# Performance work log

Measured on AMD Instinct MI355X. Metric: run time of the kernel, lower is better.

The kernel has to match this reference:

```python
import jax, jax.numpy as jnp
import numpy as np

B, H, K = 4096, 256, 16
INPUT_DIM, XPRIME_DIM = 8, 64
D = INPUT_DIM * XPRIME_DIM  # 512
LN_EPS = 1e-5


def setup_inputs() -> dict:
    key = jax.random.key(0)
    ks = jax.random.split(key, 12)
    s1 = 1.0  # Linear(1, D): fan_in=1
    sD = 1.0 / np.sqrt(D)
    sH = 1.0 / np.sqrt(H)
    return {
        "h_prev_rnn": jax.random.normal(ks[0], (B, H), jnp.float32),
        "x_l": jax.random.normal(ks[1], (B, INPUT_DIM), jnp.float32),
        "x_ext": jax.random.normal(ks[2], (B, K), jnp.float32),
        # stacked per-expert MetaNet params
        "meta_w1": jax.random.uniform(ks[3], (K, D), jnp.float32, -s1, s1),
        "meta_b1": jax.random.uniform(ks[4], (K, D), jnp.float32, -s1, s1),
        "meta_w2": jax.random.uniform(ks[5], (K, D, D), jnp.float32, -sD, sD),
        "meta_b2": jax.random.uniform(ks[6], (K, D), jnp.float32, -sD, sD),
        # gating net
        "gw1": jax.random.uniform(ks[7], (H, H), jnp.float32, -sH, sH),
        "gb1": jax.random.uniform(ks[8], (H,), jnp.float32, -sH, sH),
        "gw2": jax.random.uniform(ks[9], (H, K), jnp.float32, -sH, sH),
        "gb2": jax.random.uniform(ks[10], (K,), jnp.float32, -sH, sH),
        # LayerNorm([input_dim, xprime_dim]) affine params
        "ln_g": jnp.ones((INPUT_DIM, XPRIME_DIM), jnp.float32),
        "ln_b": jnp.zeros((INPUT_DIM, XPRIME_DIM), jnp.float32),
        "theta0": jnp.zeros((1, INPUT_DIM, XPRIME_DIM), jnp.float32),
    }


def reference(h_prev_rnn, x_l, x_ext, meta_w1, meta_b1, meta_w2, meta_b2,
              gw1, gb1, gw2, gb2, ln_g, ln_b, theta0):
    # MetaNet layer1 (Linear(1, D)): scalar input per expert -> [B, K, D]
    h1 = jnp.tanh(x_ext[:, :, None] * meta_w1[None] + meta_b1[None])
    # MetaNet layer2: per-expert DxD GEMM
    h2 = jnp.tanh(jnp.einsum('bkd,kde->bke', h1, meta_w2) + meta_b2[None])
    W = h2.reshape(h2.shape[0], K, INPUT_DIM, XPRIME_DIM)  # [B,K,i,e]
    # LayerNorm over last two dims jointly, affine
    mu = W.mean(axis=(-2, -1), keepdims=True)
    var = W.var(axis=(-2, -1), keepdims=True)
    W = (W - mu) * jax.lax.rsqrt(var + LN_EPS) * ln_g + ln_b
    # gating: softmax over experts (epoch/top_k = None path)
    logits = jnp.tanh(h_prev_rnn @ gw1 + gb1) @ gw2 + gb2
    gates = jax.nn.softmax(logits, axis=-1)  # [B, K]
    theta = jnp.einsum('bk,bkie->bie', gates, W) + theta0  # [B, i, e]
    x_prime = jnp.einsum('bi,bie->be', x_l, theta)  # [B, e]
    return (x_prime, theta)
```

## Files before the change

kernel.cpp:

```cpp
#include <hip/hip_runtime.h>
#include <stdint.h>

#define NB 4096
#define NH 256
#define NK 16
#define ND 512
#define NC 48
#define NM 48
#define RCHEB 7.0f
#define PI_F 3.14159265358979323846f
#define CCPART (NK * 2 * ND * 32)

typedef _Float16 f16;
using half8   = __attribute__((ext_vector_type(8))) _Float16;
using float4v = __attribute__((ext_vector_type(4))) float;

__device__ __forceinline__ float fast_tanh(float x) {
  float e = __builtin_amdgcn_exp2f(x * 2.88539008177793f);
  return 1.0f - 2.0f * __builtin_amdgcn_rcpf(e + 1.0f);
}

template <int CTRL>
__device__ __forceinline__ float dpp_addstep(float x) {
  int y = __builtin_amdgcn_update_dpp(0, __builtin_bit_cast(int, x),
                                      CTRL, 0xf, 0xf, true);
  return x + __builtin_bit_cast(float, y);
}
__device__ __forceinline__ float rowsum16(float x) {
  x = dpp_addstep<0xB1>(x);
  x = dpp_addstep<0x4E>(x);
  x = dpp_addstep<0x141>(x);
  x = dpp_addstep<0x140>(x);
  return x;
}

__global__ __launch_bounds__(256) void k_gs(
    const float* __restrict__ h_prev,
    const float* __restrict__ gw1, const float* __restrict__ gb1,
    const float* __restrict__ gw2, const float* __restrict__ gb2,
    const float* __restrict__ w1, const float* __restrict__ b1,
    float* __restrict__ gates, float* __restrict__ Sg, float* __restrict__ ctg) {
  __shared__ __align__(16) float sbuf[8288];
  const int t = threadIdx.x;
  const int blk = blockIdx.x;

  if (blk >= 512) {
    const int sb = blk - 512;
    const int k = sb >> 3;
    const int d0 = (sb & 7) * 64;
    if (sb == 0) {
      for (int i = t; i < NM * NC; i += 256) {
        const int m = i / 48, j = i - m * 48;
        const int r = (j * (2 * m + 1)) % 192;
        const float fac = (j == 0 ? 1.0f : 2.0f) * (1.0f / 48.0f);
        ctg[i] = cosf(PI_F * (float)r * (1.0f / 96.0f)) * fac;
      }
    }
    const int dl = t >> 2, mg = t & 3;
    const int d = d0 + dl;
    const float a = w1[k * ND + d];
    const float b = b1[k * ND + d];
    float o[12];
#pragma unroll
    for (int mi = 0; mi < 12; ++mi) {
      const int m = mg * 12 + mi;
      const float cx = cosf(PI_F * (float)(2 * m + 1) * (1.0f / 96.0f));
      o[mi] = fast_tanh(fmaf(a, RCHEB * cx, b));
    }
    float* dst = Sg + ((size_t)k * ND + d) * NM + mg * 12;
    *(float4*)&dst[0] = *(float4*)&o[0];
    *(float4*)&dst[4] = *(float4*)&o[4];
    *(float4*)&dst[8] = *(float4*)&o[8];
    return;
  }

  float* sh_h = sbuf;
  float* sh_t = sbuf + 2048;
  float* gw2t = sbuf + 4128;
  const int b0 = blk * 8;
  for (int r = 0; r < 8; ++r) sh_h[r * 256 + t] = h_prev[(b0 + r) * NH + t];
  {
    float4 gr[4];
#pragma unroll
    for (int i4 = 0; i4 < 4; ++i4) gr[i4] = *(const float4*)&gw2[t * NK + i4 * 4];
#pragma unroll
    for (int kk = 0; kk < 16; ++kk) gw2t[kk * 260 + t] = ((const float*)gr)[kk];
  }
  __syncthreads();
  float acc[8];
  const float bias = gb1[t];
#pragma unroll
  for (int r = 0; r < 8; ++r) acc[r] = bias;
  for (int i = 0; i < NH; i += 4) {
    const float w0 = gw1[(i + 0) * NH + t];
    const float w1v = gw1[(i + 1) * NH + t];
    const float w2v = gw1[(i + 2) * NH + t];
    const float w3 = gw1[(i + 3) * NH + t];
#pragma unroll
    for (int r = 0; r < 8; ++r) {
      const float4 hv = *(const float4*)&sh_h[r * 256 + i];
      acc[r] += hv.x * w0 + hv.y * w1v + hv.z * w2v + hv.w * w3;
    }
  }
#pragma unroll
  for (int r = 0; r < 8; ++r) sh_t[r * 260 + t] = fast_tanh(acc[r]);
  __syncthreads();
  if (t < 128) {
    const int r = t >> 4, k = t & 15;
    float lg = gb2[k];
#pragma unroll 8
    for (int j4 = 0; j4 < 64; ++j4) {
      const float4 tv = *(const float4*)&sh_t[r * 260 + j4 * 4];
      const float4 wv = *(const float4*)&gw2t[k * 260 + j4 * 4];
      lg += tv.x * wv.x + tv.y * wv.y + tv.z * wv.z + tv.w * wv.w;
    }
    float m = lg;
    for (int off = 1; off < 16; off <<= 1) m = fmaxf(m, __shfl_xor(m, off, 16));
    const float e = __builtin_amdgcn_exp2f((lg - m) * 1.44269504f);
    float s = e;
    for (int off = 1; off < 16; off <<= 1) s += __shfl_xor(s, off, 16);
    gates[(b0 + r) * NK + k] = e * __builtin_amdgcn_rcpf(s);
  }
}

__global__ __launch_bounds__(256) void k_coef(
    const float* __restrict__ w2, const float* __restrict__ Sg,
    const float* __restrict__ ctg, float* __restrict__ Cc) {
  __shared__ float Gl[48][68];
  const int t = threadIdx.x;
  const int blk = blockIdx.x;
  const int k = blk >> 5;
  const int e0 = ((blk >> 2) & 7) * 64;
  const int dq = blk & 3;
  const int el = t & 63;
  const int mqu = __builtin_amdgcn_readfirstlane(t >> 6);

  const float* w2p = w2 + ((size_t)k * ND + dq * 128) * ND + e0 + el;
  const float* Sp = Sg + ((size_t)k * ND + dq * 128) * NM + mqu * 12;

  float g[12];
#pragma unroll
  for (int i = 0; i < 12; ++i) g[i] = 0.f;
#pragma unroll 4
  for (int d = 0; d < 128; ++d) {
    const float wv = w2p[(size_t)d * ND];
    const float4 s0 = *(const float4*)&Sp[d * NM];
    const float4 s1 = *(const float4*)&Sp[d * NM + 4];
    const float4 s2 = *(const float4*)&Sp[d * NM + 8];
    g[0] = fmaf(s0.x, wv, g[0]);
    g[1] = fmaf(s0.y, wv, g[1]);
    g[2] = fmaf(s0.z, wv, g[2]);
    g[3] = fmaf(s0.w, wv, g[3]);
    g[4] = fmaf(s1.x, wv, g[4]);
    g[5] = fmaf(s1.y, wv, g[5]);
    g[6] = fmaf(s1.z, wv, g[6]);
    g[7] = fmaf(s1.w, wv, g[7]);
    g[8] = fmaf(s2.x, wv, g[8]);
    g[9] = fmaf(s2.y, wv, g[9]);
    g[10] = fmaf(s2.z, wv, g[10]);
    g[11] = fmaf(s2.w, wv, g[11]);
  }

#pragma unroll
  for (int mi = 0; mi < 12; ++mi) Gl[mqu * 12 + mi][el] = g[mi];
  __syncthreads();

  float cacc[12];
#pragma unroll
  for (int i = 0; i < 12; ++i) cacc[i] = 0.f;
#pragma unroll 4
  for (int m = 0; m < NM; ++m) {
    const float gv = Gl[m][el];
    const float4 c0 = *(const float4*)&ctg[m * 48 + mqu * 12];
    const float4 c1 = *(const float4*)&ctg[m * 48 + mqu * 12 + 4];
    const float4 c2 = *(const float4*)&ctg[m * 48 + mqu * 12 + 8];
    cacc[0] = fmaf(c0.x, gv, cacc[0]);
    cacc[1] = fmaf(c0.y, gv, cacc[1]);
    cacc[2] = fmaf(c0.z, gv, cacc[2]);
    cacc[3] = fmaf(c0.w, gv, cacc[3]);
    cacc[4] = fmaf(c1.x, gv, cacc[4]);
    cacc[5] = fmaf(c1.y, gv, cacc[5]);
    cacc[6] = fmaf(c1.z, gv, cacc[6]);
    cacc[7] = fmaf(c1.w, gv, cacc[7]);
    cacc[8] = fmaf(c2.x, gv, cacc[8]);
    cacc[9] = fmaf(c2.y, gv, cacc[9]);
    cacc[10] = fmaf(c2.z, gv, cacc[10]);
    cacc[11] = fmaf(c2.w, gv, cacc[11]);
  }
  float* Ccq = Cc + (size_t)dq * CCPART;
#pragma unroll
  for (int jj = 0; jj < 12; ++jj) {
    const int j = mqu * 12 + jj;
    Ccq[((size_t)(k * 2 + (j >> 5)) * ND + e0 + el) * 32 + (j & 31)] = cacc[jj];
  }
}

__global__ __launch_bounds__(256) void k_pack(
    const float* __restrict__ Cc, const float* __restrict__ b2,
    f16* __restrict__ Cbf) {
  const int idx = blockIdx.x * 256 + threadIdx.x;
  const int flat8 = idx * 8;
  const int k2 = flat8 >> 14;
  const int rem = flat8 & 16383;
  const int e = rem >> 5, o8 = rem & 31;
  const int j0 = (k2 & 1) * 32 + o8;
  f16 o[8];
  if (j0 >= 48) {
#pragma unroll
    for (int i = 0; i < 8; ++i) o[i] = (f16)0.f;
  } else {
    float v[8];
#pragma unroll
    for (int i = 0; i < 8; ++i) v[i] = 0.f;
#pragma unroll
    for (int p = 0; p < 4; ++p) {
      const float4 u0 = *(const float4*)&Cc[(size_t)p * CCPART + flat8];
      const float4 u1 = *(const float4*)&Cc[(size_t)p * CCPART + flat8 + 4];
      v[0] += u0.x; v[1] += u0.y; v[2] += u0.z; v[3] += u0.w;
      v[4] += u1.x; v[5] += u1.y; v[6] += u1.z; v[7] += u1.w;
    }
    if (((k2 & 1) == 0) && (o8 == 0)) v[0] += b2[(k2 >> 1) * ND + e];
#pragma unroll
    for (int i = 0; i < 8; ++i) o[i] = (f16)v[i];
  }
  *(uint4*)&Cbf[flat8] = *(uint4*)o;
}

__global__ __launch_bounds__(512) void k_eval(
    const f16* __restrict__ Cbf, const float* __restrict__ gates,
    const float* __restrict__ x_ext, const float* __restrict__ x_l,
    const float* __restrict__ ln_g, const float* __restrict__ ln_b,
    const float* __restrict__ theta0, float* __restrict__ out) {
  __shared__ __align__(16) char sm[40960];
  f16* Tlds = (f16*)sm;
  float (*xp)[16][68] = (float(*)[16][68])sm;
  float* lnbuf = (float*)(sm + 36864);
  float* scal  = (float*)(sm + 38144);
  float (*sx)[16] = (float(*)[16])(sm + 38400);
  float (*sg)[16] = (float(*)[16])(sm + 39424);
  float (*sxl)[8] = (float(*)[8])(sm + 40448);
  const int t = threadIdx.x;
  const int l = t & 63, wn = t >> 6;
  const int q = l >> 4, m16 = l & 15;
  const int b0 = blockIdx.x * 16;

  const f16* Bbase = Cbf + ((size_t)(wn * 64 + m16)) * 32 + q * 8;
  half8 BrA[8], BrB[8];
  auto loadB = [&](int k, half8(&dst)[8]) {
#pragma unroll
    for (int bni = 0; bni < 4; ++bni) {
      dst[bni * 2 + 0] =
          *(const half8*)(Bbase + ((size_t)(k * 2 + 0) * ND + bni * 16) * 32);
      dst[bni * 2 + 1] =
          *(const half8*)(Bbase + ((size_t)(k * 2 + 1) * ND + bni * 16) * 32);
    }
  };
  loadB(0, BrA);

  if (t < 256) {
    sx[t >> 4][t & 15] = x_ext[(b0 + (t >> 4)) * NK + (t & 15)];
    sg[t >> 4][t & 15] = gates[(b0 + (t >> 4)) * NK + (t & 15)];
  } else if (t < 384) {
    const int tt = t - 256;
    sxl[tt >> 3][tt & 7] = x_l[(b0 + (tt >> 3)) * 8 + (tt & 7)];
  }
  __syncthreads();

  if (t < 256) {
    const int k = t >> 4, row = t & 15;
    f16* T0 = &Tlds[(2 * k) * 576 + row * 36];
    f16* T1 = &Tlds[(2 * k + 1) * 576 + row * 36];
    float u = sx[row][k] * (1.0f / RCHEB);
    u = fminf(1.0f, fmaxf(-1.0f, u));
    const float u2 = u + u;
    float tp = 1.0f, tc = u;
    T0[0] = (f16)1.0f;
    T0[1] = (f16)u;
#pragma unroll
    for (int j = 2; j < 48; ++j) {
      const float tn = fmaf(u2, tc, -tp);
      tp = tc; tc = tn;
      if (j < 32) T0[j] = (f16)tn; else T1[j - 32] = (f16)tn;
    }
#pragma unroll
    for (int j = 48; j < 64; ++j) T1[j - 32] = (f16)0.f;
  }
  __syncthreads();

  float lng[4], lnb[4];
#pragma unroll
  for (int bni = 0; bni < 4; ++bni) {
    const int col = wn * 64 + bni * 16 + m16;
    lng[bni] = ln_g[col];
    lnb[bni] = ln_b[col];
  }

  float th[4][4];
#pragma unroll
  for (int bni = 0; bni < 4; ++bni)
#pragma unroll
    for (int rr = 0; rr < 4; ++rr) th[bni][rr] = 0.f;

  const f16* Abase = Tlds + m16 * 36 + q * 8;
  const float4v z = {0.f, 0.f, 0.f, 0.f};

  float4v acc[4];
  float s[4], s2[4];

  auto stepA = [&](int k, const half8(&Br)[8]) {
    const half8 a0 = *(const half8*)(Abase + (2 * k) * 576);
    const half8 a1 = *(const half8*)(Abase + (2 * k + 1) * 576);
#pragma unroll
    for (int bni = 0; bni < 4; ++bni) {
      acc[bni] = __builtin_amdgcn_mfma_f32_16x16x32_f16(a0, Br[2 * bni], z, 0, 0, 0);
      acc[bni] = __builtin_amdgcn_mfma_f32_16x16x32_f16(a1, Br[2 * bni + 1],
                                                        acc[bni], 0, 0, 0);
    }
#pragma unroll
    for (int rr = 0; rr < 4; ++rr) { s[rr] = 0.f; s2[rr] = 0.f; }
#pragma unroll
    for (int bni = 0; bni < 4; ++bni)
#pragma unroll
      for (int rr = 0; rr < 4; ++rr) {
        const float v = fast_tanh(acc[bni][rr]);
        acc[bni][rr] = v;
        s[rr] += v;
        s2[rr] = fmaf(v, v, s2[rr]);
      }
#pragma unroll
    for (int rr = 0; rr < 4; ++rr) {
      s[rr] = rowsum16(s[rr]);
      s2[rr] = rowsum16(s2[rr]);
    }
    if (m16 == 0) {
#pragma unroll
      for (int rr = 0; rr < 4; ++rr)
        *(float2*)&lnbuf[(q * 4 + rr) * 20 + wn * 2] = make_float2(s[rr], s2[rr]);
    }
  };
  auto scalc = [&](int k) {
    if (wn == 0 && l < 16) {
      const int row = l;
      const float4 p0 = *(const float4*)&lnbuf[row * 20 + 0];
      const float4 p1 = *(const float4*)&lnbuf[row * 20 + 4];
      const float4 p2 = *(const float4*)&lnbuf[row * 20 + 8];
      const float4 p3 = *(const float4*)&lnbuf[row * 20 + 12];
      const float S1 = p0.x + p0.z + p1.x + p1.z + p2.x + p2.z + p3.x + p3.z;
      const float S2 = p0.y + p0.w + p1.y + p1.w + p2.y + p2.w + p3.y + p3.w;
      const float mu = S1 * (1.0f / 512.0f);
      const float var = fmaf(S2, 1.0f / 512.0f, -mu * mu);
      const float rs = __builtin_amdgcn_rsqf(var + 1e-5f);
      const float gate = sg[row][k];
      const float A = gate * rs;
      *(float4*)&scal[row * 4] = make_float4(A, A * mu, gate, 0.0f);
    }
  };
  auto apply = [&]() {
#pragma unroll
    for (int rr = 0; rr < 4; ++rr) {
      const int row = q * 4 + rr;
      const float4 sc = *(const float4*)&scal[row * 4];
      const float A = sc.x, M = sc.y, gate = sc.z;
#pragma unroll
      for (int bni = 0; bni < 4; ++bni)
        th[bni][rr] = fmaf(A * lng[bni], acc[bni][rr],
                       fmaf(-M, lng[bni],
                        fmaf(gate, lnb[bni], th[bni][rr])));
    }
  };

  for (int kp = 0; kp < 8; ++kp) {
    stepA(2 * kp, BrA);
    loadB(2 * kp + 1, BrB);
    __syncthreads();
    scalc(2 * kp);
    __syncthreads();
    apply();
    stepA(2 * kp + 1, BrB);
    if (kp < 7) loadB(2 * kp + 2, BrA);
    __syncthreads();
    scalc(2 * kp + 1);
    __syncthreads();
    apply();
  }

  float* thbase = out + (size_t)NB * 64;
#pragma unroll
  for (int bni = 0; bni < 4; ++bni) {
    const int col = wn * 64 + bni * 16 + m16;
    const float t0v = theta0[col];
#pragma unroll
    for (int rr = 0; rr < 4; ++rr) {
      const float o = th[bni][rr] + t0v;
      th[bni][rr] = o;
      thbase[(size_t)(b0 + q * 4 + rr) * ND + col] = o;
    }
  }
  __syncthreads();
#pragma unroll
  for (int rr = 0; rr < 4; ++rr) {
    const int row = q * 4 + rr;
    const float xlw = sxl[row][wn];
#pragma unroll
    for (int bni = 0; bni < 4; ++bni)
      xp[wn][row][bni * 16 + m16] = xlw * th[bni][rr];
  }
  __syncthreads();
  {
    const int idx = t * 2;
    const int row = idx >> 6, ec = idx & 63;
    float2 r = {0.f, 0.f};
#pragma unroll
    for (int w8 = 0; w8 < 8; ++w8) {
      const float2 p = *(const float2*)&xp[w8][row][ec];
      r.x += p.x;
      r.y += p.y;
    }
    *(float2*)&out[(size_t)(b0 + row) * 64 + ec] = r;
  }
}

extern "C" void kernel_launch(void* const* d_in, const int* in_sizes, int n_in,
                              void* d_out, int out_size, void* d_ws, size_t ws_size,
                              hipStream_t stream) {
  const float* h_prev = (const float*)d_in[0];
  const float* x_l    = (const float*)d_in[1];
  const float* x_ext  = (const float*)d_in[2];
  const float* mw1    = (const float*)d_in[3];
  const float* mb1    = (const float*)d_in[4];
  const float* mw2    = (const float*)d_in[5];
  const float* mb2    = (const float*)d_in[6];
  const float* gw1    = (const float*)d_in[7];
  const float* gb1    = (const float*)d_in[8];
  const float* gw2    = (const float*)d_in[9];
  const float* gb2    = (const float*)d_in[10];
  const float* ln_g   = (const float*)d_in[11];
  const float* ln_b   = (const float*)d_in[12];
  const float* th0    = (const float*)d_in[13];
  float* out = (float*)d_out;

  char* ws = (char*)d_ws;
  float* gates = (float*)ws;
  f16* Cbf     = (f16*)(ws + 0x40000);
  float* Cc    = (float*)(ws + 0x140000);
  float* Sg    = (float*)(ws + 0x940000);
  float* ctg   = (float*)(ws + 0xB00000);

  hipLaunchKernelGGL(k_gs, dim3(640), dim3(256), 0, stream,
                     h_prev, gw1, gb1, gw2, gb2, mw1, mb1, gates, Sg, ctg);
  hipLaunchKernelGGL(k_coef, dim3(512), dim3(256), 0, stream,
                     mw2, Sg, ctg, Cc);
  hipLaunchKernelGGL(k_pack, dim3(256), dim3(256), 0, stream,
                     Cc, mb2, Cbf);
  hipLaunchKernelGGL(k_eval, dim3(256), dim3(512), 0, stream,
                     Cbf, gates, x_ext, x_l, ln_g, ln_b, th0, out);
}
```

Before: 161.7 us.

## Fuse coefficient split-K and pack kernels, pair expert steps in eval loop

The Chebyshev coefficient kernel now covers the full 512-long reduction per block with 512 threads and writes packed fp16 coefficients plus bias directly. This removes the fp32 partial-sum buffer and the separate pack kernel launch. The Sg and cosine tables are padded to a stride of 4 per group of 3 so each thread issues one float4 load. In the eval kernel, two experts' MFMA steps run back to back with separate accumulators and double-buffered LayerNorm stats, halving the number of barrier pairs per expert pair. The cost is less parallelism in k_coef: only 256 blocks each run a 512-step serial loop, and more registers are needed in k_eval.

```diff
diff --git a/kernel.cpp b/kernel.cpp
--- a/kernel.cpp
+++ b/kernel.cpp
@@ -9,7 +9,6 @@
 #define NM 48
 #define RCHEB 7.0f
 #define PI_F 3.14159265358979323846f
-#define CCPART (NK * 2 * ND * 32)
 
 typedef _Float16 f16;
 using half8   = __attribute__((ext_vector_type(8))) _Float16;
@@ -53,7 +52,7 @@
         const int m = i / 48, j = i - m * 48;
         const int r = (j * (2 * m + 1)) % 192;
         const float fac = (j == 0 ? 1.0f : 2.0f) * (1.0f / 48.0f);
-        ctg[i] = cosf(PI_F * (float)r * (1.0f / 96.0f)) * fac;
+        ctg[m * 64 + (j / 3) * 4 + (j % 3)] = cosf(PI_F * (float)r * (1.0f / 96.0f)) * fac;
       }
     }
     const int dl = t >> 2, mg = t & 3;
@@ -67,10 +66,11 @@
       const float cx = cosf(PI_F * (float)(2 * m + 1) * (1.0f / 96.0f));
       o[mi] = fast_tanh(fmaf(a, RCHEB * cx, b));
     }
-    float* dst = Sg + ((size_t)k * ND + d) * NM + mg * 12;
-    *(float4*)&dst[0] = *(float4*)&o[0];
-    *(float4*)&dst[4] = *(float4*)&o[4];
-    *(float4*)&dst[8] = *(float4*)&o[8];
+    float* dst = Sg + ((size_t)k * ND + d) * 64 + mg * 16;
+#pragma unroll
+    for (int g4 = 0; g4 < 4; ++g4)
+      *(float4*)&dst[g4 * 4] =
+          make_float4(o[g4 * 3], o[g4 * 3 + 1], o[g4 * 3 + 2], 0.f);
     return;
   }
 
@@ -123,107 +123,57 @@
   }
 }
 
-__global__ __launch_bounds__(256) void k_coef(
+__global__ __launch_bounds__(512) void k_coef(
     const float* __restrict__ w2, const float* __restrict__ Sg,
-    const float* __restrict__ ctg, float* __restrict__ Cc) {
-  __shared__ float Gl[48][68];
+    const float* __restrict__ ctg, const float* __restrict__ b2,
+    f16* __restrict__ Cbf) {
+  __shared__ float Gl[48][36];
   const int t = threadIdx.x;
-  const int blk = blockIdx.x;
-  const int k = blk >> 5;
-  const int e0 = ((blk >> 2) & 7) * 64;
-  const int dq = blk & 3;
-  const int el = t & 63;
-  const int mqu = __builtin_amdgcn_readfirstlane(t >> 6);
-
-  const float* w2p = w2 + ((size_t)k * ND + dq * 128) * ND + e0 + el;
-  const float* Sp = Sg + ((size_t)k * ND + dq * 128) * NM + mqu * 12;
-
-  float g[12];
-#pragma unroll
-  for (int i = 0; i < 12; ++i) g[i] = 0.f;
-#pragma unroll 4
-  for (int d = 0; d < 128; ++d) {
+  const int k = blockIdx.x >> 4;
+  const int e0 = (blockIdx.x & 15) * 32;
+  const int el = t & 31;
+  const int mq = t >> 5;
+
+  const float* w2p = w2 + (size_t)k * ND * ND + e0 + el;
+  const float* Sp = Sg + (size_t)k * ND * 64 + mq * 4;
+
+  float g0 = 0.f, g1 = 0.f, g2 = 0.f;
+#pragma unroll 8
+  for (int d = 0; d < ND; ++d) {
     const float wv = w2p[(size_t)d * ND];
-    const float4 s0 = *(const float4*)&Sp[d * NM];
-    const float4 s1 = *(const float4*)&Sp[d * NM + 4];
-    const float4 s2 = *(const float4*)&Sp[d * NM + 8];
-    g[0] = fmaf(s0.x, wv, g[0]);
-    g[1] = fmaf(s0.y, wv, g[1]);
-    g[2] = fmaf(s0.z, wv, g[2]);
-    g[3] = fmaf(s0.w, wv, g[3]);
-    g[4] = fmaf(s1.x, wv, g[4]);
-    g[5] = fmaf(s1.y, wv, g[5]);
-    g[6] = fmaf(s1.z, wv, g[6]);
-    g[7] = fmaf(s1.w, wv, g[7]);
-    g[8] = fmaf(s2.x, wv, g[8]);
-    g[9] = fmaf(s2.y, wv, g[9]);
-    g[10] = fmaf(s2.z, wv, g[10]);
-    g[11] = fmaf(s2.w, wv, g[11]);
-  }
-
-#pragma unroll
-  for (int mi = 0; mi < 12; ++mi) Gl[mqu * 12 + mi][el] = g[mi];
-  __syncthreads();
-
-  float cacc[12];
-#pragma unroll
-  for (int i = 0; i < 12; ++i) cacc[i] = 0.f;
+    const float4 s = *(const float4*)&Sp[d * 64];
+    g0 = fmaf(s.x, wv, g0);
+    g1 = fmaf(s.y, wv, g1);
+    g2 = fmaf(s.z, wv, g2);
+  }
+  Gl[mq * 3 + 0][el] = g0;
+  Gl[mq * 3 + 1][el] = g1;
+  Gl[mq * 3 + 2][el] = g2;
+  __syncthreads();
+
+  const int jq = mq;
+  float c0 = 0.f, c1 = 0.f, c2 = 0.f;
 #pragma unroll 4
   for (int m = 0; m < NM; ++m) {
     const float gv = Gl[m][el];
-    const float4 c0 = *(const float4*)&ctg[m * 48 + mqu * 12];
-    const float4 c1 = *(const float4*)&ctg[m * 48 + mqu * 12 + 4];
-    const float4 c2 = *(const float4*)&ctg[m * 48 + mqu * 12 + 8];
-    cacc[0] = fmaf(c0.x, gv, cacc[0]);
-    cacc[1] = fmaf(c0.y, gv, cacc[1]);
-    cacc[2] = fmaf(c0.z, gv, cacc[2]);
-    cacc[3] = fmaf(c0.w, gv, cacc[3]);
-    cacc[4] = fmaf(c1.x, gv, cacc[4]);
-    cacc[5] = fmaf(c1.y, gv, cacc[5]);
-    cacc[6] = fmaf(c1.z, gv, cacc[6]);
-    cacc[7] = fmaf(c1.w, gv, cacc[7]);
-    cacc[8] = fmaf(c2.x, gv, cacc[8]);
-    cacc[9] = fmaf(c2.y, gv, cacc[9]);
-    cacc[10] = fmaf(c2.z, gv, cacc[10]);
-    cacc[11] = fmaf(c2.w, gv, cacc[11]);
-  }
-  float* Ccq = Cc + (size_t)dq * CCPART;
-#pragma unroll
-  for (int jj = 0; jj < 12; ++jj) {
-    const int j = mqu * 12 + jj;
-    Ccq[((size_t)(k * 2 + (j >> 5)) * ND + e0 + el) * 32 + (j & 31)] = cacc[jj];
-  }
-}
-
-__global__ __launch_bounds__(256) void k_pack(
-    const float* __restrict__ Cc, const float* __restrict__ b2,
-    f16* __restrict__ Cbf) {
-  const int idx = blockIdx.x * 256 + threadIdx.x;
-  const int flat8 = idx * 8;
-  const int k2 = flat8 >> 14;
-  const int rem = flat8 & 16383;
-  const int e = rem >> 5, o8 = rem & 31;
-  const int j0 = (k2 & 1) * 32 + o8;
-  f16 o[8];
-  if (j0 >= 48) {
-#pragma unroll
-    for (int i = 0; i < 8; ++i) o[i] = (f16)0.f;
-  } else {
-    float v[8];
-#pragma unroll
-    for (int i = 0; i < 8; ++i) v[i] = 0.f;
-#pragma unroll
-    for (int p = 0; p < 4; ++p) {
-      const float4 u0 = *(const float4*)&Cc[(size_t)p * CCPART + flat8];
-      const float4 u1 = *(const float4*)&Cc[(size_t)p * CCPART + flat8 + 4];
-      v[0] += u0.x; v[1] += u0.y; v[2] += u0.z; v[3] += u0.w;
-      v[4] += u1.x; v[5] += u1.y; v[6] += u1.z; v[7] += u1.w;
-    }
-    if (((k2 & 1) == 0) && (o8 == 0)) v[0] += b2[(k2 >> 1) * ND + e];
-#pragma unroll
-    for (int i = 0; i < 8; ++i) o[i] = (f16)v[i];
-  }
-  *(uint4*)&Cbf[flat8] = *(uint4*)o;
+    const float4 cc = *(const float4*)&ctg[m * 64 + jq * 4];
+    c0 = fmaf(cc.x, gv, c0);
+    c1 = fmaf(cc.y, gv, c1);
+    c2 = fmaf(cc.z, gv, c2);
+  }
+  const int e = e0 + el;
+  const float b2v = b2[k * ND + e];
+  const float vals[3] = {c0, c1, c2};
+#pragma unroll
+  for (int jj = 0; jj < 3; ++jj) {
+    const int j = jq * 3 + jj;
+    const float v = vals[jj] + (j == 0 ? b2v : 0.f);
+    Cbf[((size_t)(k * 2 + (j >> 5)) * ND + e) * 32 + (j & 31)] = (f16)v;
+  }
+  {
+    const int j = 48 + mq;
+    Cbf[((size_t)(k * 2 + 1) * ND + e) * 32 + (j - 32)] = (f16)0.f;
+  }
 }
 
 __global__ __launch_bounds__(512) void k_eval(
@@ -231,14 +181,14 @@
     const float* __restrict__ x_ext, const float* __restrict__ x_l,
     const float* __restrict__ ln_g, const float* __restrict__ ln_b,
     const float* __restrict__ theta0, float* __restrict__ out) {
-  __shared__ __align__(16) char sm[40960];
+  __shared__ __align__(16) char sm[42496];
   f16* Tlds = (f16*)sm;
   float (*xp)[16][68] = (float(*)[16][68])sm;
   float* lnbuf = (float*)(sm + 36864);
-  float* scal  = (float*)(sm + 38144);
-  float (*sx)[16] = (float(*)[16])(sm + 38400);
-  float (*sg)[16] = (float(*)[16])(sm + 39424);
-  float (*sxl)[8] = (float(*)[8])(sm + 40448);
+  float* scal  = (float*)(sm + 39424);
+  float (*sx)[16] = (float(*)[16])(sm + 39936);
+  float (*sg)[16] = (float(*)[16])(sm + 40960);
+  float (*sxl)[8] = (float(*)[8])(sm + 41984);
   const int t = threadIdx.x;
   const int l = t & 63, wn = t >> 6;
   const int q = l >> 4, m16 = l & 15;
@@ -256,6 +206,7 @@
     }
   };
   loadB(0, BrA);
+  loadB(1, BrB);
 
   if (t < 256) {
     sx[t >> 4][t & 15] = x_ext[(b0 + (t >> 4)) * NK + (t & 15)];
@@ -304,10 +255,7 @@
   const f16* Abase = Tlds + m16 * 36 + q * 8;
   const float4v z = {0.f, 0.f, 0.f, 0.f};
 
-  float4v acc[4];
-  float s[4], s2[4];
-
-  auto stepA = [&](int k, const half8(&Br)[8]) {
+  auto stepA = [&](int k, const half8(&Br)[8], float4v(&acc)[4]) {
     const half8 a0 = *(const half8*)(Abase + (2 * k) * 576);
     const half8 a1 = *(const half8*)(Abase + (2 * k + 1) * 576);
 #pragma unroll
@@ -316,6 +264,7 @@
       acc[bni] = __builtin_amdgcn_mfma_f32_16x16x32_f16(a1, Br[2 * bni + 1],
                                                         acc[bni], 0, 0, 0);
     }
+    float s[4], s2[4];
 #pragma unroll
     for (int rr = 0; rr < 4; ++rr) { s[rr] = 0.f; s2[rr] = 0.f; }
 #pragma unroll
@@ -335,31 +284,33 @@
     if (m16 == 0) {
 #pragma unroll
       for (int rr = 0; rr < 4; ++rr)
-        *(float2*)&lnbuf[(q * 4 + rr) * 20 + wn * 2] = make_float2(s[rr], s2[rr]);
+        *(float2*)&lnbuf[(k & 1) * 320 + (q * 4 + rr) * 20 + wn * 2] =
+            make_float2(s[rr], s2[rr]);
     }
   };
-  auto scalc = [&](int k) {
-    if (wn == 0 && l < 16) {
-      const int row = l;
-      const float4 p0 = *(const float4*)&lnbuf[row * 20 + 0];
-      const float4 p1 = *(const float4*)&lnbuf[row * 20 + 4];
-      const float4 p2 = *(const float4*)&lnbuf[row * 20 + 8];
-      const float4 p3 = *(const float4*)&lnbuf[row * 20 + 12];
+  auto scalc2 = [&](int kp) {
+    if (t < 32) {
+      const int ks = t >> 4, row = t & 15;
+      const float* lb = lnbuf + ks * 320 + row * 20;
+      const float4 p0 = *(const float4*)&lb[0];
+      const float4 p1 = *(const float4*)&lb[4];
+      const float4 p2 = *(const float4*)&lb[8];
+      const float4 p3 = *(const float4*)&lb[12];
       const float S1 = p0.x + p0.z + p1.x + p1.z + p2.x + p2.z + p3.x + p3.z;
       const float S2 = p0.y + p0.w + p1.y + p1.w + p2.y + p2.w + p3.y + p3.w;
       const float mu = S1 * (1.0f / 512.0f);
       const float var = fmaf(S2, 1.0f / 512.0f, -mu * mu);
       const float rs = __builtin_amdgcn_rsqf(var + 1e-5f);
-      const float gate = sg[row][k];
+      const float gate = sg[row][2 * kp + ks];
       const float A = gate * rs;
-      *(float4*)&scal[row * 4] = make_float4(A, A * mu, gate, 0.0f);
+      *(float4*)&scal[ks * 64 + row * 4] = make_float4(A, A * mu, gate, 0.0f);
     }
   };
-  auto apply = [&]() {
+  auto apply = [&](const float4v(&acc)[4], int slot) {
 #pragma unroll
     for (int rr = 0; rr < 4; ++rr) {
       const int row = q * 4 + rr;
-      const float4 sc = *(const float4*)&scal[row * 4];
+      const float4 sc = *(const float4*)&scal[slot * 64 + row * 4];
       const float A = sc.x, M = sc.y, gate = sc.z;
 #pragma unroll
       for (int bni = 0; bni < 4; ++bni)
@@ -369,19 +320,17 @@
     }
   };
 
+  float4v accA[4], accB[4];
   for (int kp = 0; kp < 8; ++kp) {
-    stepA(2 * kp, BrA);
-    loadB(2 * kp + 1, BrB);
+    stepA(2 * kp, BrA, accA);
+    if (kp < 7) loadB(2 * kp + 2, BrA);
+    stepA(2 * kp + 1, BrB, accB);
+    if (kp < 7) loadB(2 * kp + 3, BrB);
     __syncthreads();
-    scalc(2 * kp);
+    scalc2(kp);
     __syncthreads();
-    apply();
-    stepA(2 * kp + 1, BrB);
-    if (kp < 7) loadB(2 * kp + 2, BrA);
-    __syncthreads();
-    scalc(2 * kp + 1);
-    __syncthreads();
-    apply();
+    apply(accA, 0);
+    apply(accB, 1);
   }
 
   float* thbase = out + (size_t)NB * 64;
@@ -442,16 +391,13 @@
   char* ws = (char*)d_ws;
   float* gates = (float*)ws;
   f16* Cbf     = (f16*)(ws + 0x40000);
-  float* Cc    = (float*)(ws + 0x140000);
-  float* Sg    = (float*)(ws + 0x940000);
-  float* ctg   = (float*)(ws + 0xB00000);
+  float* Sg    = (float*)(ws + 0x140000);
+  float* ctg   = (float*)(ws + 0x340000);
 
   hipLaunchKernelGGL(k_gs, dim3(640), dim3(256), 0, stream,
                      h_prev, gw1, gb1, gw2, gb2, mw1, mb1, gates, Sg, ctg);
-  hipLaunchKernelGGL(k_coef, dim3(512), dim3(256), 0, stream,
-                     mw2, Sg, ctg, Cc);
-  hipLaunchKernelGGL(k_pack, dim3(256), dim3(256), 0, stream,
-                     Cc, mb2, Cbf);
+  hipLaunchKernelGGL(k_coef, dim3(256), dim3(512), 0, stream,
+                     mw2, Sg, ctg, mb2, Cbf);
   hipLaunchKernelGGL(k_eval, dim3(256), dim3(512), 0, stream,
                      Cbf, gates, x_ext, x_l, ln_g, ln_b, th0, out);
 }
```

After: 180.3 us. 1.12x slower.

## Batch two experts per barrier pair with double-buffered LN stats and deeper prefetch

Applied to the files above, without the earlier changes.

The expert loop now computes MFMA and tanh for two experts back to back into separate accumulators. It then reduces both experts' LayerNorm statistics in one scalc pass using double-buffered lnbuf/scal slots, which halves the number of __syncthreads per expert pair. B-fragment loads are issued one expert further ahead. In exchange, register pressure rises from a second accumulator set and an extra in-flight B buffer, and shared memory grows slightly.

```diff
diff --git a/kernel.cpp b/kernel.cpp
--- a/kernel.cpp
+++ b/kernel.cpp
@@ -231,14 +231,14 @@
     const float* __restrict__ x_ext, const float* __restrict__ x_l,
     const float* __restrict__ ln_g, const float* __restrict__ ln_b,
     const float* __restrict__ theta0, float* __restrict__ out) {
-  __shared__ __align__(16) char sm[40960];
+  __shared__ __align__(16) char sm[42496];
   f16* Tlds = (f16*)sm;
   float (*xp)[16][68] = (float(*)[16][68])sm;
   float* lnbuf = (float*)(sm + 36864);
-  float* scal  = (float*)(sm + 38144);
-  float (*sx)[16] = (float(*)[16])(sm + 38400);
-  float (*sg)[16] = (float(*)[16])(sm + 39424);
-  float (*sxl)[8] = (float(*)[8])(sm + 40448);
+  float* scal  = (float*)(sm + 39424);
+  float (*sx)[16] = (float(*)[16])(sm + 39936);
+  float (*sg)[16] = (float(*)[16])(sm + 40960);
+  float (*sxl)[8] = (float(*)[8])(sm + 41984);
   const int t = threadIdx.x;
   const int l = t & 63, wn = t >> 6;
   const int q = l >> 4, m16 = l & 15;
@@ -256,6 +256,7 @@
     }
   };
   loadB(0, BrA);
+  loadB(1, BrB);
 
   if (t < 256) {
     sx[t >> 4][t & 15] = x_ext[(b0 + (t >> 4)) * NK + (t & 15)];
@@ -304,10 +305,7 @@
   const f16* Abase = Tlds + m16 * 36 + q * 8;
   const float4v z = {0.f, 0.f, 0.f, 0.f};
 
-  float4v acc[4];
-  float s[4], s2[4];
-
-  auto stepA = [&](int k, const half8(&Br)[8]) {
+  auto stepA = [&](int k, const half8(&Br)[8], float4v(&acc)[4]) {
     const half8 a0 = *(const half8*)(Abase + (2 * k) * 576);
     const half8 a1 = *(const half8*)(Abase + (2 * k + 1) * 576);
 #pragma unroll
@@ -316,6 +314,7 @@
       acc[bni] = __builtin_amdgcn_mfma_f32_16x16x32_f16(a1, Br[2 * bni + 1],
                                                         acc[bni], 0, 0, 0);
     }
+    float s[4], s2[4];
 #pragma unroll
     for (int rr = 0; rr < 4; ++rr) { s[rr] = 0.f; s2[rr] = 0.f; }
 #pragma unroll
@@ -335,31 +334,33 @@
     if (m16 == 0) {
 #pragma unroll
       for (int rr = 0; rr < 4; ++rr)
-        *(float2*)&lnbuf[(q * 4 + rr) * 20 + wn * 2] = make_float2(s[rr], s2[rr]);
+        *(float2*)&lnbuf[(k & 1) * 320 + (q * 4 + rr) * 20 + wn * 2] =
+            make_float2(s[rr], s2[rr]);
     }
   };
-  auto scalc = [&](int k) {
-    if (wn == 0 && l < 16) {
-      const int row = l;
-      const float4 p0 = *(const float4*)&lnbuf[row * 20 + 0];
-      const float4 p1 = *(const float4*)&lnbuf[row * 20 + 4];
-      const float4 p2 = *(const float4*)&lnbuf[row * 20 + 8];
-      const float4 p3 = *(const float4*)&lnbuf[row * 20 + 12];
+  auto scalc2 = [&](int kp) {
+    if (t < 32) {
+      const int ks = t >> 4, row = t & 15;
+      const float* lb = lnbuf + ks * 320 + row * 20;
+      const float4 p0 = *(const float4*)&lb[0];
+      const float4 p1 = *(const float4*)&lb[4];
+      const float4 p2 = *(const float4*)&lb[8];
+      const float4 p3 = *(const float4*)&lb[12];
       const float S1 = p0.x + p0.z + p1.x + p1.z + p2.x + p2.z + p3.x + p3.z;
       const float S2 = p0.y + p0.w + p1.y + p1.w + p2.y + p2.w + p3.y + p3.w;
       const float mu = S1 * (1.0f / 512.0f);
       const float var = fmaf(S2, 1.0f / 512.0f, -mu * mu);
       const float rs = __builtin_amdgcn_rsqf(var + 1e-5f);
-      const float gate = sg[row][k];
+      const float gate = sg[row][2 * kp + ks];
       const float A = gate * rs;
-      *(float4*)&scal[row * 4] = make_float4(A, A * mu, gate, 0.0f);
+      *(float4*)&scal[ks * 64 + row * 4] = make_float4(A, A * mu, gate, 0.0f);
     }
   };
-  auto apply = [&]() {
+  auto apply = [&](const float4v(&acc)[4], int slot) {
 #pragma unroll
     for (int rr = 0; rr < 4; ++rr) {
       const int row = q * 4 + rr;
-      const float4 sc = *(const float4*)&scal[row * 4];
+      const float4 sc = *(const float4*)&scal[slot * 64 + row * 4];
       const float A = sc.x, M = sc.y, gate = sc.z;
 #pragma unroll
       for (int bni = 0; bni < 4; ++bni)
@@ -369,19 +370,17 @@
     }
   };
 
+  float4v accA[4], accB[4];
   for (int kp = 0; kp < 8; ++kp) {
-    stepA(2 * kp, BrA);
-    loadB(2 * kp + 1, BrB);
+    stepA(2 * kp, BrA, accA);
+    if (kp < 7) loadB(2 * kp + 2, BrA);
+    stepA(2 * kp + 1, BrB, accB);
+    if (kp < 7) loadB(2 * kp + 3, BrB);
     __syncthreads();
-    scalc(2 * kp);
+    scalc2(kp);
     __syncthreads();
-    apply();
-    stepA(2 * kp + 1, BrB);
-    if (kp < 7) loadB(2 * kp + 2, BrA);
-    __syncthreads();
-    scalc(2 * kp + 1);
-    __syncthreads();
-    apply();
+    apply(accA, 0);
+    apply(accB, 1);
   }
 
   float* thbase = out + (size_t)NB * 64;
```

Result: no change. 161.3 us (-0.2%).
